# Kernel tuning notes

Hardware: AMD Instinct MI355X
Metric: run time of the kernel (lower is better)

Reference implementation:

```python
import jax, jax.numpy as jnp
import numpy as np

S, B, D, NH = 4096, 4, 1024, 16


def _unitnorm(v):
    # v / ||v||_2 along last dim (matches torch.norm(v, dim=-1))
    return v / jnp.linalg.norm(v, axis=-1, keepdims=True)


def setup_inputs() -> dict:
    key = jax.random.key(0)
    ks = jax.random.split(key, 9)
    scale = 1.0 / np.sqrt(D)
    inp = {
        "h": jax.random.normal(ks[0], (S, B, D), dtype=jnp.float32),
        "Wq_w": jax.random.normal(ks[1], (D, D), dtype=jnp.float32) * scale,
        "Wq_b": jax.random.normal(ks[2], (D,), dtype=jnp.float32) * scale,
        "Wk_w": jax.random.normal(ks[3], (D, D), dtype=jnp.float32) * scale,
        "Wk_b": jax.random.normal(ks[4], (D,), dtype=jnp.float32) * scale,
        "Wv_w": jax.random.normal(ks[5], (D, D), dtype=jnp.float32) * scale,
        "Wv_b": jax.random.normal(ks[6], (D,), dtype=jnp.float32) * scale,
        "Wo_w": jax.random.normal(ks[7], (D, D), dtype=jnp.float32) * scale,
        "Wo_b": jax.random.normal(ks[8], (D,), dtype=jnp.float32) * scale,
        "nhead": NH,
    }
    return inp


def reference(h, Wq_w, Wq_b, Wk_w, Wk_b, Wv_w, Wv_b, Wo_w, Wo_b, nhead):
    s, b, d = h.shape
    dh = d // nhead

    def proj(W, bias):
        # torch nn.Linear: x @ W.T + b, then split heads -> [S,B,NH,dh]
        return (h @ W.T + bias).reshape(s, b, nhead, dh)

    k = jax.nn.elu(_unitnorm(proj(Wk_w, Wk_b)))  # unitelu
    v = proj(Wv_w, Wv_b)
    q = _unitnorm(proj(Wq_w, Wq_b))  # sigma = unitnorm (default)

    # Linear-attention state: sum of outer products over the whole sequence
    A = jnp.einsum('sbnq,sbnv->bnvq', k, v)  # [B,NH,dh,dh]
    out = jnp.einsum('sbnq,bnvq->sbnv', q, A).reshape(s, b, d)
    out = out @ Wo_w.T + Wo_b
    return out, k, q
```

## Files before the change

kernel.cpp:

```cpp
#include <hip/hip_runtime.h>
#include <hip/hip_bf16.h>
#include <math.h>

#define S_LEN 4096
#define B_SZ  4
#define D_DIM 1024
#define NHEAD 16
#define R_ROWS (S_LEN * B_SZ)

#define AS1 __attribute__((address_space(1)))
#define AS3 __attribute__((address_space(3)))

typedef __bf16 bf16_t;
typedef __attribute__((ext_vector_type(8))) __bf16 bf16x8;
typedef __attribute__((ext_vector_type(4))) __bf16 bf16x4;
typedef __attribute__((ext_vector_type(4))) float  f32x4;

#define MFMA16 __builtin_amdgcn_mfma_f32_16x16x32_bf16

__device__ __forceinline__ void gload16(const bf16_t* g, bf16_t* l) {
  __builtin_amdgcn_global_load_lds((const AS1 unsigned int*)g,
                                   (AS3 unsigned int*)l, 16, 0, 0);
}
__device__ __forceinline__ void hard_barrier() {
  asm volatile("s_barrier" ::: "memory");
}

__global__ void k_cvt(const float* __restrict__ src, bf16_t* __restrict__ dst, int n) {
  int i = (blockIdx.x * 256 + threadIdx.x) * 4;
  if (i >= n) return;
  f32x4 v = *(const f32x4*)(src + i);
  bf16x4 o;
  o[0] = (bf16_t)v[0]; o[1] = (bf16_t)v[1]; o[2] = (bf16_t)v[2]; o[3] = (bf16_t)v[3];
  *(bf16x4*)(dst + i) = o;
}

template <typename SHA, typename SHB>
__device__ __forceinline__ void gemm_core_256x128(
    const bf16_t* __restrict__ A, const bf16_t* __restrict__ B,
    int row0, int col0, SHA& sA, SHB& sB, f32x4 acc[4][4])
{
  const int tid  = threadIdx.x;
  const int wave = tid >> 6, lane = tid & 63;
  const int lr = lane & 15, lg = lane >> 4;
  const int wr = wave >> 1, wn = wave & 1;
  const int srow = tid >> 3, schunk = tid & 7;
  const int sch_swz = schunk ^ (srow & 7);

  auto stageA = [&](int buf, int k0, int j) {
    gload16(&A[(size_t)(row0 + j * 64 + srow) * D_DIM + k0 + sch_swz * 8],
            &sA[buf][(j * 64 + wave * 8) * 64]);
  };
  auto stageB = [&](int buf, int k0, int j) {
    gload16(&B[(size_t)(col0 + j * 64 + srow) * D_DIM + k0 + sch_swz * 8],
            &sB[buf][(j * 64 + wave * 8) * 64]);
  };
  auto rdA = [&](int buf, int m, int kk) -> bf16x8 {
    const int r = wr * 64 + m * 16 + lr;
    const int ch = ((kk >> 3) + lg) ^ (r & 7);
    return *(const bf16x8*)&sA[buf][r * 64 + ch * 8];
  };
  auto rdB = [&](int buf, int n, int kk) -> bf16x8 {
    const int r = wn * 64 + n * 16 + lr;
    const int ch = ((kk >> 3) + lg) ^ (r & 7);
    return *(const bf16x8*)&sB[buf][r * 64 + ch * 8];
  };

  #pragma unroll
  for (int m = 0; m < 4; m++)
    #pragma unroll
    for (int n = 0; n < 4; n++)
      #pragma unroll
      for (int r = 0; r < 4; r++) acc[m][n][r] = 0.f;

  #pragma unroll
  for (int j = 0; j < 4; ++j) stageA(0, 0, j);
  #pragma unroll
  for (int j = 0; j < 2; ++j) stageB(0, 0, j);
  #pragma unroll
  for (int j = 0; j < 4; ++j) stageA(1, 64, j);
  #pragma unroll
  for (int j = 0; j < 2; ++j) stageB(1, 64, j);
  asm volatile("s_waitcnt vmcnt(6)" ::: "memory");
  hard_barrier();

  for (int t = 0; t < 16; ++t) {
    const int c  = t % 3;
    const int cn = (t + 2) % 3;
    const int kn = (t + 2) * 64;
    const bool st = (t < 14);

    bf16x8 bfr[4][2];
    #pragma unroll
    for (int n = 0; n < 4; ++n) { bfr[n][0] = rdB(c, n, 0); bfr[n][1] = rdB(c, n, 32); }
    bf16x8 a00 = rdA(c, 0, 0), a01 = rdA(c, 0, 32);
    bf16x8 a10 = rdA(c, 1, 0), a11 = rdA(c, 1, 32);
    if (st) { stageA(cn, kn, 0); stageA(cn, kn, 1); stageB(cn, kn, 0); }
    hard_barrier();
    asm volatile("s_waitcnt lgkmcnt(0)" ::: "memory");
    __builtin_amdgcn_sched_barrier(0);
    __builtin_amdgcn_s_setprio(1);
    #pragma unroll
    for (int n = 0; n < 4; ++n) {
      acc[0][n] = MFMA16(a00, bfr[n][0], acc[0][n], 0, 0, 0);
      acc[0][n] = MFMA16(a01, bfr[n][1], acc[0][n], 0, 0, 0);
      acc[1][n] = MFMA16(a10, bfr[n][0], acc[1][n], 0, 0, 0);
      acc[1][n] = MFMA16(a11, bfr[n][1], acc[1][n], 0, 0, 0);
    }
    __builtin_amdgcn_s_setprio(0);
    hard_barrier();

    bf16x8 a20 = rdA(c, 2, 0), a21 = rdA(c, 2, 32);
    bf16x8 a30 = rdA(c, 3, 0), a31 = rdA(c, 3, 32);
    if (st) { stageA(cn, kn, 2); stageA(cn, kn, 3); stageB(cn, kn, 1); }
    hard_barrier();
    asm volatile("s_waitcnt lgkmcnt(0)" ::: "memory");
    __builtin_amdgcn_sched_barrier(0);
    __builtin_amdgcn_s_setprio(1);
    #pragma unroll
    for (int n = 0; n < 4; ++n) {
      acc[2][n] = MFMA16(a20, bfr[n][0], acc[2][n], 0, 0, 0);
      acc[2][n] = MFMA16(a21, bfr[n][1], acc[2][n], 0, 0, 0);
      acc[3][n] = MFMA16(a30, bfr[n][0], acc[3][n], 0, 0, 0);
      acc[3][n] = MFMA16(a31, bfr[n][1], acc[3][n], 0, 0, 0);
    }
    __builtin_amdgcn_s_setprio(0);
    if (t < 14)       asm volatile("s_waitcnt vmcnt(6)" ::: "memory");
    else if (t == 14) asm volatile("s_waitcnt vmcnt(0)" ::: "memory");
    hard_barrier();
  }
}

__global__ __launch_bounds__(512, 2) void k_proj(
    const bf16_t* __restrict__ hB, const bf16_t* __restrict__ Wcat,
    const float* __restrict__ bq, const float* __restrict__ bk, const float* __restrict__ bv,
    bf16_t* __restrict__ outVb, float* __restrict__ outK, float* __restrict__ outQ,
    bf16_t* __restrict__ qBm)
{
  __shared__ bf16_t sA[3][256 * 64];
  __shared__ bf16_t sB[3][128 * 64];

  const int tid  = threadIdx.x;
  const int wave = tid >> 6, lane = tid & 63;
  const int lr = lane & 15, lg = lane >> 4;
  const int wr = wave >> 1, wn = wave & 1;
  const int row0 = blockIdx.x * 256;
  const int bn   = blockIdx.y;

  f32x4 acc[4][4];
  gemm_core_256x128(hB, Wcat, row0, bn * 128, sA, sB, acc);

  const int sec = bn >> 3;
  const int hc0 = (bn & 7) * 128 + wn * 64;
  const float* bias = (sec == 0) ? bq : (sec == 1 ? bk : bv);
  float bvv[4];
  #pragma unroll
  for (int n = 0; n < 4; n++) bvv[n] = bias[hc0 + n * 16 + lr];

  #pragma unroll
  for (int m = 0; m < 4; ++m) {
    #pragma unroll
    for (int r = 0; r < 4; ++r) {
      const int gm = row0 + wr * 64 + m * 16 + lg * 4 + r;
      float v[4];
      float ss = 0.f;
      #pragma unroll
      for (int n = 0; n < 4; n++) {
        v[n] = acc[m][n][r] + bvv[n];
        ss += v[n] * v[n];
      }
      if (sec == 2) {
        #pragma unroll
        for (int n = 0; n < 4; n++)
          outVb[(size_t)gm * D_DIM + hc0 + n * 16 + lr] = (bf16_t)v[n];
      } else {
        #pragma unroll
        for (int msk = 1; msk < 16; msk <<= 1) ss += __shfl_xor(ss, msk);
        const float rs = 1.0f / sqrtf(ss);
        if (sec == 0) {
          const size_t qrow = (size_t)(gm & 3) * S_LEN + (gm >> 2);
          #pragma unroll
          for (int n = 0; n < 4; n++) {
            const float qn = v[n] * rs;
            outQ[(size_t)gm * D_DIM + hc0 + n * 16 + lr] = qn;
            qBm[qrow * D_DIM + hc0 + n * 16 + lr] = (bf16_t)qn;
          }
        } else {
          #pragma unroll
          for (int n = 0; n < 4; n++) {
            float kn = v[n] * rs;
            kn = kn > 0.f ? kn : expm1f(kn);
            outK[(size_t)gm * D_DIM + hc0 + n * 16 + lr] = kn;
          }
        }
      }
    }
  }
}

__global__ __launch_bounds__(256) void k_state(
    const float* __restrict__ Kf, const bf16_t* __restrict__ Vb,
    float* __restrict__ Apart)
{
  const int bn = blockIdx.x;
  const int ch = blockIdx.y;
  const int b = bn >> 4, n = bn & 15;
  const int tid = threadIdx.x;
  const int ti = tid >> 4, tj = tid & 15;

  __shared__ float sV[32][64];
  __shared__ float sK[32][64];

  float acc[4][4];
  #pragma unroll
  for (int i = 0; i < 4; i++)
    #pragma unroll
    for (int j = 0; j < 4; j++) acc[i][j] = 0.f;

  const int rr = tid >> 3, cc = (tid & 7) * 8;
  for (int s0 = ch * 512; s0 < ch * 512 + 512; s0 += 32) {
    const size_t g = (size_t)((s0 + rr) * B_SZ + b) * D_DIM + n * 64 + cc;
    bf16x8 v8 = *(const bf16x8*)&Vb[g];
    #pragma unroll
    for (int e = 0; e < 8; e++) sV[rr][cc + e] = (float)v8[e];
    *(f32x4*)&sK[rr][cc]     = *(const f32x4*)&Kf[g];
    *(f32x4*)&sK[rr][cc + 4] = *(const f32x4*)&Kf[g + 4];
    __syncthreads();
    #pragma unroll
    for (int ss = 0; ss < 32; ss++) {
      f32x4 vv = *(const f32x4*)&sV[ss][ti * 4];
      f32x4 kk = *(const f32x4*)&sK[ss][tj * 4];
      #pragma unroll
      for (int i = 0; i < 4; i++)
        #pragma unroll
        for (int j = 0; j < 4; j++)
          acc[i][j] = fmaf(vv[i], kk[j], acc[i][j]);
    }
    __syncthreads();
  }
  float* ap = Apart + ((size_t)ch * 64 + bn) * 4096;
  #pragma unroll
  for (int i = 0; i < 4; i++)
    #pragma unroll
    for (int j = 0; j < 4; j++)
      ap[(ti * 4 + i) * 64 + tj * 4 + j] = acc[i][j];
}

__global__ __launch_bounds__(256) void k_combine(
    const float* __restrict__ Apart, const bf16_t* __restrict__ WoB,
    bf16_t* __restrict__ Ct)
{
  const int bn = blockIdx.x;
  const int dp = blockIdx.y;
  const int b = bn >> 4, n = bn & 15;
  const int tid = threadIdx.x;
  const int ti = tid >> 4, tj = tid & 15;

  __shared__ float sAm[64][65];
  __shared__ float sW[64][65];

  #pragma unroll
  for (int p = 0; p < 16; p++) {
    const int idx = tid + p * 256;
    float s = 0.f;
    #pragma unroll
    for (int c2 = 0; c2 < 8; c2++)
      s += Apart[((size_t)c2 * 64 + bn) * 4096 + idx];
    sAm[idx >> 6][idx & 63] = s;
  }
  {
    const int r = tid >> 2, cv = (tid & 3) * 16;
    bf16x8 w0 = *(const bf16x8*)&WoB[(size_t)(dp * 64 + r) * D_DIM + n * 64 + cv];
    bf16x8 w1 = *(const bf16x8*)&WoB[(size_t)(dp * 64 + r) * D_DIM + n * 64 + cv + 8];
    #pragma unroll
    for (int e = 0; e < 8; e++) {
      sW[r][cv + e]     = (float)w0[e];
      sW[r][cv + 8 + e] = (float)w1[e];
    }
  }
  __syncthreads();

  float acc[4][4];
  #pragma unroll
  for (int i = 0; i < 4; i++)
    #pragma unroll
    for (int j = 0; j < 4; j++) acc[i][j] = 0.f;

  for (int dv = 0; dv < 64; dv++) {
    float w[4], a[4];
    #pragma unroll
    for (int i = 0; i < 4; i++) w[i] = sW[ti * 4 + i][dv];
    #pragma unroll
    for (int j = 0; j < 4; j++) a[j] = sAm[dv][tj * 4 + j];
    #pragma unroll
    for (int i = 0; i < 4; i++)
      #pragma unroll
      for (int j = 0; j < 4; j++)
        acc[i][j] = fmaf(w[i], a[j], acc[i][j]);
  }
  #pragma unroll
  for (int i = 0; i < 4; i++)
    #pragma unroll
    for (int j = 0; j < 4; j++)
      Ct[((size_t)b * D_DIM + dp * 64 + ti * 4 + i) * D_DIM + n * 64 + tj * 4 + j] =
          (bf16_t)acc[i][j];
}

__global__ __launch_bounds__(512, 2) void k_final(
    const bf16_t* __restrict__ qBm, const bf16_t* __restrict__ Ct,
    const float* __restrict__ bo, float* __restrict__ outO)
{
  __shared__ bf16_t sA[3][256 * 64];
  __shared__ bf16_t sB[3][128 * 64];

  const int tid  = threadIdx.x;
  const int wave = tid >> 6, lane = tid & 63;
  const int lr = lane & 15, lg = lane >> 4;
  const int wr = wave >> 1, wn = wave & 1;
  const int b    = blockIdx.z;
  const int row0 = blockIdx.x * 256;
  const int col0 = blockIdx.y * 128;

  f32x4 acc[4][4];
  gemm_core_256x128(qBm + (size_t)b * S_LEN * D_DIM, Ct + (size_t)b * D_DIM * D_DIM,
                    row0, col0, sA, sB, acc);

  #pragma unroll
  for (int m = 0; m < 4; ++m) {
    #pragma unroll
    for (int r = 0; r < 4; ++r) {
      const int gs = row0 + wr * 64 + m * 16 + lg * 4 + r;
      #pragma unroll
      for (int n = 0; n < 4; n++) {
        const int col = col0 + wn * 64 + n * 16 + lr;
        outO[((size_t)gs * B_SZ + b) * D_DIM + col] = acc[m][n][r] + bo[col];
      }
    }
  }
}

extern "C" void kernel_launch(void* const* d_in, const int* in_sizes, int n_in,
                              void* d_out, int out_size, void* d_ws, size_t ws_size,
                              hipStream_t stream) {
  (void)in_sizes; (void)n_in; (void)out_size; (void)ws_size;
  const float* h  = (const float*)d_in[0];
  const float* Wq = (const float*)d_in[1];
  const float* bq = (const float*)d_in[2];
  const float* Wk = (const float*)d_in[3];
  const float* bk = (const float*)d_in[4];
  const float* Wv = (const float*)d_in[5];
  const float* bv = (const float*)d_in[6];
  const float* Wo = (const float*)d_in[7];
  const float* bo = (const float*)d_in[8];

  float* out0 = (float*)d_out;
  float* outK = out0 + (size_t)R_ROWS * D_DIM;
  float* outQ = outK + (size_t)R_ROWS * D_DIM;
  bf16_t* vB  = (bf16_t*)d_out;

  char* ws = (char*)d_ws;
  bf16_t* hB    = (bf16_t*)ws;
  bf16_t* Ct    = (bf16_t*)ws;
  bf16_t* Wcat  = (bf16_t*)(ws + 33554432);
  bf16_t* WoB   = (bf16_t*)(ws + 33554432 + 6291456);
  float*  Apart = (float*)(ws + 41943040);
  bf16_t* qBm   = (bf16_t*)(ws + 50331648);

  const int nH = R_ROWS * D_DIM;
  const int nW = D_DIM * D_DIM;
  k_cvt<<<nH / 1024, 256, 0, stream>>>(h, hB, nH);
  k_cvt<<<nW / 1024, 256, 0, stream>>>(Wq, Wcat, nW);
  k_cvt<<<nW / 1024, 256, 0, stream>>>(Wk, Wcat + nW, nW);
  k_cvt<<<nW / 1024, 256, 0, stream>>>(Wv, Wcat + 2 * nW, nW);
  k_cvt<<<nW / 1024, 256, 0, stream>>>(Wo, WoB, nW);

  k_proj<<<dim3(R_ROWS / 256, 24), 512, 0, stream>>>(hB, Wcat, bq, bk, bv,
                                                     vB, outK, outQ, qBm);
  k_state<<<dim3(64, 8), 256, 0, stream>>>(outK, vB, Apart);
  k_combine<<<dim3(64, 16), 256, 0, stream>>>(Apart, WoB, Ct);
  k_final<<<dim3(S_LEN / 256, D_DIM / 128, B_SZ), 512, 0, stream>>>(qBm, Ct, bo, out0);
}
```

Baseline: 277.5 us.

## Switch GEMM core to 256x256 tiles with BK=32 and 2x4 wave layout

Replaces the 256x128 block tile (BK=64) with a 256x256 tile (BK=32) shared by the projection and final GEMMs. Waves are arranged 2x4 with 128x64 per-wave sub-tiles, LDS offsets are precomputed, and a 4-chunk XOR swizzle replaces the 8-chunk one. Each block now reuses the A tile across twice as many output columns, which halves the projection grid and cuts global/LDS traffic per FLOP. In exchange, per-thread accumulators double (more register pressure, possibly lower occupancy under launch_bounds(512,2)), K iterations double, and the grid has fewer blocks.

```diff
diff --git a/kernel.cpp b/kernel.cpp
--- a/kernel.cpp
+++ b/kernel.cpp
@@ -35,98 +35,90 @@
   *(bf16x4*)(dst + i) = o;
 }
 
-template <typename SHA, typename SHB>
-__device__ __forceinline__ void gemm_core_256x128(
+__device__ __forceinline__ void gemm_core_256(
     const bf16_t* __restrict__ A, const bf16_t* __restrict__ B,
-    int row0, int col0, SHA& sA, SHB& sB, f32x4 acc[4][4])
+    int row0, int col0,
+    bf16_t (&sA)[3][8192], bf16_t (&sB)[3][8192], f32x4 (&acc)[8][4])
 {
   const int tid  = threadIdx.x;
   const int wave = tid >> 6, lane = tid & 63;
   const int lr = lane & 15, lg = lane >> 4;
-  const int wr = wave >> 1, wn = wave & 1;
-  const int srow = tid >> 3, schunk = tid & 7;
-  const int sch_swz = schunk ^ (srow & 7);
+  const int wr = wave >> 2, wn = wave & 3;
+  const int grow = tid >> 2;
+  const int gch  = (tid & 3) ^ (grow & 3);
 
   auto stageA = [&](int buf, int k0, int j) {
-    gload16(&A[(size_t)(row0 + j * 64 + srow) * D_DIM + k0 + sch_swz * 8],
-            &sA[buf][(j * 64 + wave * 8) * 64]);
+    gload16(&A[(size_t)(row0 + j * 128 + grow) * D_DIM + k0 + gch * 8],
+            &sA[buf][(j * 512 + wave * 64) * 8]);
   };
   auto stageB = [&](int buf, int k0, int j) {
-    gload16(&B[(size_t)(col0 + j * 64 + srow) * D_DIM + k0 + sch_swz * 8],
-            &sB[buf][(j * 64 + wave * 8) * 64]);
+    gload16(&B[(size_t)(col0 + j * 128 + grow) * D_DIM + k0 + gch * 8],
+            &sB[buf][(j * 512 + wave * 64) * 8]);
   };
-  auto rdA = [&](int buf, int m, int kk) -> bf16x8 {
-    const int r = wr * 64 + m * 16 + lr;
-    const int ch = ((kk >> 3) + lg) ^ (r & 7);
-    return *(const bf16x8*)&sA[buf][r * 64 + ch * 8];
-  };
-  auto rdB = [&](int buf, int n, int kk) -> bf16x8 {
+
+  int aoff[8], boff[4];
+  #pragma unroll
+  for (int m = 0; m < 8; m++) {
+    const int r = wr * 128 + m * 16 + lr;
+    aoff[m] = r * 32 + (lg ^ (r & 3)) * 8;
+  }
+  #pragma unroll
+  for (int n = 0; n < 4; n++) {
     const int r = wn * 64 + n * 16 + lr;
-    const int ch = ((kk >> 3) + lg) ^ (r & 7);
-    return *(const bf16x8*)&sB[buf][r * 64 + ch * 8];
-  };
-
-  #pragma unroll
-  for (int m = 0; m < 4; m++)
+    boff[n] = r * 32 + (lg ^ (r & 3)) * 8;
+  }
+
+  #pragma unroll
+  for (int m = 0; m < 8; m++)
     #pragma unroll
     for (int n = 0; n < 4; n++)
       #pragma unroll
       for (int r = 0; r < 4; r++) acc[m][n][r] = 0.f;
 
-  #pragma unroll
-  for (int j = 0; j < 4; ++j) stageA(0, 0, j);
-  #pragma unroll
-  for (int j = 0; j < 2; ++j) stageB(0, 0, j);
-  #pragma unroll
-  for (int j = 0; j < 4; ++j) stageA(1, 64, j);
-  #pragma unroll
-  for (int j = 0; j < 2; ++j) stageB(1, 64, j);
-  asm volatile("s_waitcnt vmcnt(6)" ::: "memory");
+  stageA(0, 0, 0); stageA(0, 0, 1); stageB(0, 0, 0); stageB(0, 0, 1);
+  stageA(1, 32, 0); stageA(1, 32, 1); stageB(1, 32, 0); stageB(1, 32, 1);
+  asm volatile("s_waitcnt vmcnt(4)" ::: "memory");
   hard_barrier();
 
-  for (int t = 0; t < 16; ++t) {
+  for (int t = 0; t < 32; ++t) {
     const int c  = t % 3;
     const int cn = (t + 2) % 3;
-    const int kn = (t + 2) * 64;
-    const bool st = (t < 14);
-
-    bf16x8 bfr[4][2];
-    #pragma unroll
-    for (int n = 0; n < 4; ++n) { bfr[n][0] = rdB(c, n, 0); bfr[n][1] = rdB(c, n, 32); }
-    bf16x8 a00 = rdA(c, 0, 0), a01 = rdA(c, 0, 32);
-    bf16x8 a10 = rdA(c, 1, 0), a11 = rdA(c, 1, 32);
-    if (st) { stageA(cn, kn, 0); stageA(cn, kn, 1); stageB(cn, kn, 0); }
+    const int kn = (t + 2) * 32;
+    const bool st = (t < 30);
+
+    bf16x8 bfr[4], afr[4];
+    #pragma unroll
+    for (int n = 0; n < 4; ++n) bfr[n] = *(const bf16x8*)&sB[c][boff[n]];
+    #pragma unroll
+    for (int m = 0; m < 4; ++m) afr[m] = *(const bf16x8*)&sA[c][aoff[m]];
+    if (st) { stageA(cn, kn, 0); stageA(cn, kn, 1); }
     hard_barrier();
     asm volatile("s_waitcnt lgkmcnt(0)" ::: "memory");
     __builtin_amdgcn_sched_barrier(0);
     __builtin_amdgcn_s_setprio(1);
     #pragma unroll
-    for (int n = 0; n < 4; ++n) {
-      acc[0][n] = MFMA16(a00, bfr[n][0], acc[0][n], 0, 0, 0);
-      acc[0][n] = MFMA16(a01, bfr[n][1], acc[0][n], 0, 0, 0);
-      acc[1][n] = MFMA16(a10, bfr[n][0], acc[1][n], 0, 0, 0);
-      acc[1][n] = MFMA16(a11, bfr[n][1], acc[1][n], 0, 0, 0);
-    }
+    for (int m = 0; m < 4; ++m)
+      #pragma unroll
+      for (int n = 0; n < 4; ++n)
+        acc[m][n] = MFMA16(afr[m], bfr[n], acc[m][n], 0, 0, 0);
     __builtin_amdgcn_s_setprio(0);
     hard_barrier();
 
-    bf16x8 a20 = rdA(c, 2, 0), a21 = rdA(c, 2, 32);
-    bf16x8 a30 = rdA(c, 3, 0), a31 = rdA(c, 3, 32);
-    if (st) { stageA(cn, kn, 2); stageA(cn, kn, 3); stageB(cn, kn, 1); }
+    #pragma unroll
+    for (int m = 0; m < 4; ++m) afr[m] = *(const bf16x8*)&sA[c][aoff[m + 4]];
+    if (st) { stageB(cn, kn, 0); stageB(cn, kn, 1); }
     hard_barrier();
     asm volatile("s_waitcnt lgkmcnt(0)" ::: "memory");
     __builtin_amdgcn_sched_barrier(0);
     __builtin_amdgcn_s_setprio(1);
     #pragma unroll
-    for (int n = 0; n < 4; ++n) {
-      acc[2][n] = MFMA16(a20, bfr[n][0], acc[2][n], 0, 0, 0);
-      acc[2][n] = MFMA16(a21, bfr[n][1], acc[2][n], 0, 0, 0);
-      acc[3][n] = MFMA16(a30, bfr[n][0], acc[3][n], 0, 0, 0);
-      acc[3][n] = MFMA16(a31, bfr[n][1], acc[3][n], 0, 0, 0);
-    }
+    for (int m = 0; m < 4; ++m)
+      #pragma unroll
+      for (int n = 0; n < 4; ++n)
+        acc[m + 4][n] = MFMA16(afr[m], bfr[n], acc[m + 4][n], 0, 0, 0);
     __builtin_amdgcn_s_setprio(0);
-    if (t < 14)       asm volatile("s_waitcnt vmcnt(6)" ::: "memory");
-    else if (t == 14) asm volatile("s_waitcnt vmcnt(0)" ::: "memory");
+    if (t < 30)       asm volatile("s_waitcnt vmcnt(4)" ::: "memory");
+    else if (t == 30) asm volatile("s_waitcnt vmcnt(0)" ::: "memory");
     hard_barrier();
   }
 }
@@ -137,31 +129,31 @@
     bf16_t* __restrict__ outVb, float* __restrict__ outK, float* __restrict__ outQ,
     bf16_t* __restrict__ qBm)
 {
-  __shared__ bf16_t sA[3][256 * 64];
-  __shared__ bf16_t sB[3][128 * 64];
+  __shared__ bf16_t sA[3][8192];
+  __shared__ bf16_t sB[3][8192];
 
   const int tid  = threadIdx.x;
   const int wave = tid >> 6, lane = tid & 63;
   const int lr = lane & 15, lg = lane >> 4;
-  const int wr = wave >> 1, wn = wave & 1;
+  const int wr = wave >> 2, wn = wave & 3;
   const int row0 = blockIdx.x * 256;
-  const int bn   = blockIdx.y;
-
-  f32x4 acc[4][4];
-  gemm_core_256x128(hB, Wcat, row0, bn * 128, sA, sB, acc);
-
-  const int sec = bn >> 3;
-  const int hc0 = (bn & 7) * 128 + wn * 64;
+  const int by   = blockIdx.y;
+
+  f32x4 acc[8][4];
+  gemm_core_256(hB, Wcat, row0, by * 256, sA, sB, acc);
+
+  const int sec = by >> 2;
+  const int hc0 = (by & 3) * 256 + wn * 64;
   const float* bias = (sec == 0) ? bq : (sec == 1 ? bk : bv);
   float bvv[4];
   #pragma unroll
   for (int n = 0; n < 4; n++) bvv[n] = bias[hc0 + n * 16 + lr];
 
   #pragma unroll
-  for (int m = 0; m < 4; ++m) {
+  for (int m = 0; m < 8; ++m) {
     #pragma unroll
     for (int r = 0; r < 4; ++r) {
-      const int gm = row0 + wr * 64 + m * 16 + lg * 4 + r;
+      const int gm = row0 + wr * 128 + m * 16 + lg * 4 + r;
       float v[4];
       float ss = 0.f;
       #pragma unroll
@@ -310,26 +302,26 @@
     const bf16_t* __restrict__ qBm, const bf16_t* __restrict__ Ct,
     const float* __restrict__ bo, float* __restrict__ outO)
 {
-  __shared__ bf16_t sA[3][256 * 64];
-  __shared__ bf16_t sB[3][128 * 64];
+  __shared__ bf16_t sA[3][8192];
+  __shared__ bf16_t sB[3][8192];
 
   const int tid  = threadIdx.x;
   const int wave = tid >> 6, lane = tid & 63;
   const int lr = lane & 15, lg = lane >> 4;
-  const int wr = wave >> 1, wn = wave & 1;
+  const int wr = wave >> 2, wn = wave & 3;
   const int b    = blockIdx.z;
   const int row0 = blockIdx.x * 256;
-  const int col0 = blockIdx.y * 128;
-
-  f32x4 acc[4][4];
-  gemm_core_256x128(qBm + (size_t)b * S_LEN * D_DIM, Ct + (size_t)b * D_DIM * D_DIM,
-                    row0, col0, sA, sB, acc);
-
-  #pragma unroll
-  for (int m = 0; m < 4; ++m) {
+  const int col0 = blockIdx.y * 256;
+
+  f32x4 acc[8][4];
+  gemm_core_256(qBm + (size_t)b * S_LEN * D_DIM, Ct + (size_t)b * D_DIM * D_DIM,
+                row0, col0, sA, sB, acc);
+
+  #pragma unroll
+  for (int m = 0; m < 8; ++m) {
     #pragma unroll
     for (int r = 0; r < 4; ++r) {
-      const int gs = row0 + wr * 64 + m * 16 + lg * 4 + r;
+      const int gs = row0 + wr * 128 + m * 16 + lg * 4 + r;
       #pragma unroll
       for (int n = 0; n < 4; n++) {
         const int col = col0 + wn * 64 + n * 16 + lr;
@@ -374,9 +366,9 @@
   k_cvt<<<nW / 1024, 256, 0, stream>>>(Wv, Wcat + 2 * nW, nW);
   k_cvt<<<nW / 1024, 256, 0, stream>>>(Wo, WoB, nW);
 
-  k_proj<<<dim3(R_ROWS / 256, 24), 512, 0, stream>>>(hB, Wcat, bq, bk, bv,
+  k_proj<<<dim3(R_ROWS / 256, 12), 512, 0, stream>>>(hB, Wcat, bq, bk, bv,
                                                      vB, outK, outQ, qBm);
   k_state<<<dim3(64, 8), 256, 0, stream>>>(outK, vB, Apart);
   k_combine<<<dim3(64, 16), 256, 0, stream>>>(Apart, WoB, Ct);
-  k_final<<<dim3(S_LEN / 256, D_DIM / 128, B_SZ), 512, 0, stream>>>(qBm, Ct, bo, out0);
-}
+  k_final<<<dim3(S_LEN / 256, D_DIM / 256, B_SZ), 512, 0, stream>>>(qBm, Ct, bo, out0);
+}
```

Measured after the change: 265.3 us. -4.4%, faster.
